# Optimization experiments

Measured on AMD Instinct MI355X. Metric: run time of the kernel, lower is better.

Reference implementation:

```python
import jax, jax.numpy as jnp
import numpy as np

T, B, H, V = 128, 32, 1024, 32000


def setup_inputs() -> dict:
    key = jax.random.key(0)
    ks = jax.random.split(key, 8)
    scale = 1.0 / np.sqrt(H)
    return {
        "input": jax.random.normal(ks[0], (T, B, H), dtype=jnp.float32),
        "hidden": jnp.zeros((B, H), dtype=jnp.float32),
        "w_ic": jax.random.uniform(ks[1], (H, H), jnp.float32, -scale, scale),
        "w_ix": jax.random.uniform(ks[2], (H, H), jnp.float32, -scale, scale),
        "w_fc": jax.random.uniform(ks[3], (H, H), jnp.float32, -scale, scale),
        "w_fx": jax.random.uniform(ks[4], (H, H), jnp.float32, -scale, scale),
        "b_i": jnp.zeros((H,), dtype=jnp.float32),
        "b_f": jnp.zeros((H,), dtype=jnp.float32),
        "W_out": jax.random.uniform(ks[5], (V, H), jnp.float32, -scale, scale),
        "b_out": jnp.zeros((V,), dtype=jnp.float32),
    }


def reference(input, hidden, w_ic, w_ix, w_fc, w_fx, b_i, b_f, W_out, b_out):
    # Precompute input projections for all timesteps: [T, B, H]
    ix = jnp.einsum("tbh,kh->tbk", input, w_ix)
    fx = jnp.einsum("tbh,kh->tbk", input, w_fx)

    def step(c, xs):
        ix_t, fx_t, x_t = xs
        i_t = jax.nn.sigmoid(c @ w_ic.T + b_i + ix_t)
        f_t = jax.nn.sigmoid(c @ w_fc.T + b_f + fx_t)
        c_new = i_t * x_t + f_t * c  # RAN gated-additive update
        return c_new, c_new

    hidden_final, outputs = jax.lax.scan(step, hidden, (ix, fx, input))
    logits = jnp.einsum("tbh,vh->tbv", outputs, W_out) + b_out
    log_probs = jax.nn.log_softmax(logits, axis=-1)
    return log_probs, hidden_final
```

## Files before the change

### kernel.cpp

```cpp
#include <hip/hip_runtime.h>

typedef __attribute__((ext_vector_type(4))) float f32x4;
typedef __attribute__((ext_vector_type(8))) short bf16x8;
typedef __attribute__((ext_vector_type(4))) unsigned u32x4;

#define T_DIM 128
#define B_DIM 32
#define H_DIM 1024
#define V_DIM 32000
#define MROWS 4096
#define NBLK 64
#define PUBSTEP 32768
#define WSTRIDE 1028
#define GBK 32

__device__ __forceinline__ ushort f2bf(float f){
  union { float f; unsigned u; } x; x.f = f;
  unsigned u = x.u;
  unsigned r = (u + 0x7fffu + ((u >> 16) & 1u)) >> 16;
  return (ushort)r;
}
__device__ __forceinline__ float bf2f(ushort h){
  union { unsigned u; float f; } x; x.u = ((unsigned)h) << 16;
  return x.f;
}

__device__ __forceinline__ void async_copy16(void* lds, const void* g){
  __builtin_amdgcn_global_load_lds((const __attribute__((address_space(1))) void*)g,
                                   (__attribute__((address_space(3))) void*)lds, 16, 0, 0);
}

__global__ void cast_bf16_kernel(const float* __restrict__ s, ushort* __restrict__ d, int n4){
  int stride = gridDim.x * blockDim.x;
  for (int i = blockIdx.x*blockDim.x + threadIdx.x; i < n4; i += stride){
    float4 v = ((const float4*)s)[i];
    ushort4 o = make_ushort4(f2bf(v.x), f2bf(v.y), f2bf(v.z), f2bf(v.w));
    ((ushort4*)d)[i] = o;
  }
}

__global__ void cast_split_kernel(const float* __restrict__ s, ushort* __restrict__ dh,
                                  ushort* __restrict__ dl, int n4){
  int stride = gridDim.x * blockDim.x;
  for (int i = blockIdx.x*blockDim.x + threadIdx.x; i < n4; i += stride){
    float4 v = ((const float4*)s)[i];
    ushort4 h = make_ushort4(f2bf(v.x), f2bf(v.y), f2bf(v.z), f2bf(v.w));
    ushort4 l = make_ushort4(f2bf(v.x - bf2f(h.x)), f2bf(v.y - bf2f(h.y)),
                             f2bf(v.z - bf2f(h.z)), f2bf(v.w - bf2f(h.w)));
    ((ushort4*)dh)[i] = h;
    ((ushort4*)dl)[i] = l;
  }
}

__global__ __launch_bounds__(256) void gemm_bt_plain(
    const ushort* __restrict__ A, const ushort* __restrict__ B,
    float* __restrict__ C, int N, int K, int NTN)
{
  __shared__ ushort lA[128*32];
  __shared__ ushort lB[128*32];
  int tid = threadIdx.x;
  int lane = tid & 63, wid = tid >> 6;
  int tm = blockIdx.x / NTN, tn = blockIdx.x % NTN;
  int row0 = tm << 7, col0 = tn << 7;

  f32x4 acc[4][4] = {};

  auto stage = [&](const ushort* __restrict__ g, ushort* l, int r0, int k0){
    int c = wid << 1;
    const ushort* s0 = g + (size_t)(r0 + (c<<4) + (lane>>2))*K + k0 + ((lane&3)<<3);
    async_copy16(l + (c<<9), s0);
    async_copy16(l + ((c+1)<<9), s0 + (size_t)16*K);
  };

  int nk = K >> 5;
  stage(A, lA, row0, 0);
  stage(B, lB, col0, 0);
  int wm = (wid >> 1) << 6, wn = (wid & 1) << 6;
  int kg = (lane >> 4) << 3;
  int ar = lane & 15;

  for (int kt = 0; kt < nk; ++kt){
    __syncthreads();
    bf16x8 af[4], bfr[4];
    #pragma unroll
    for (int mi = 0; mi < 4; ++mi) af[mi]  = *(const bf16x8*)&lA[(wm + mi*16 + ar)*32 + kg];
    #pragma unroll
    for (int ni = 0; ni < 4; ++ni) bfr[ni] = *(const bf16x8*)&lB[(wn + ni*16 + ar)*32 + kg];
    #pragma unroll
    for (int mi = 0; mi < 4; ++mi)
      #pragma unroll
      for (int ni = 0; ni < 4; ++ni)
        acc[mi][ni] = __builtin_amdgcn_mfma_f32_16x16x32_bf16(af[mi], bfr[ni], acc[mi][ni], 0, 0, 0);
    if (kt + 1 < nk){
      __syncthreads();
      stage(A, lA, row0, (kt+1) << 5);
      stage(B, lB, col0, (kt+1) << 5);
    }
  }

  int rr = (lane >> 4) << 2;
  #pragma unroll
  for (int mi = 0; mi < 4; ++mi)
    #pragma unroll
    for (int ni = 0; ni < 4; ++ni){
      int r  = row0 + wm + mi*16 + rr;
      int cc = col0 + wn + ni*16 + ar;
      #pragma unroll
      for (int q = 0; q < 4; ++q)
        C[(size_t)(r + q) * N + cc] = acc[mi][ni][q];
    }
}

__global__ __launch_bounds__(512) void gemm256(
    const ushort* __restrict__ A, const ushort* __restrict__ B,
    float* __restrict__ C, const float* __restrict__ bias,
    float* __restrict__ pmax, float* __restrict__ psum)
{
  __shared__ ushort lA[4][256*GBK];
  __shared__ ushort lB[4][256*GBK];
  __shared__ float redm[2][4][128], reds[2][4][128];

  const int K = 1024, N = V_DIM, NTN = 125, NT = 32;
  int tid = threadIdx.x, lane = tid & 63, wid = tid >> 6;
  int wm = wid >> 2, wn = wid & 3;
  int bid = blockIdx.x;
  int xcd = bid & 7, id = bid >> 3;
  int tm = (xcd << 1) | (id & 1);
  int tn = id >> 1;
  int row0 = tm << 8, col0 = tn << 8;
  int ar = lane & 15, kg = (lane >> 4) << 3;

  auto STAGE = [&](int slot, int kt){
    int k0 = kt << 5;
    #pragma unroll
    for (int j = 0; j < 2; ++j){
      int u = j*512 + tid;
      int r = u >> 2, p = u & 3;
      int g = p ^ ((r >> 1) & 3);
      int rA = row0 + r, k = k0 + (g << 3);
      const ushort* sA = A + ((size_t)(rA>>5)<<15) + ((size_t)(k>>4)<<9) + ((rA&31)<<4) + (k&15);
      async_copy16(&lA[slot][u<<3], sA);
    }
    #pragma unroll
    for (int j = 0; j < 2; ++j){
      int u = j*512 + tid;
      int r = u >> 2, p = u & 3;
      int g = p ^ ((r >> 1) & 3);
      const ushort* sB = B + (size_t)(col0 + r)*K + k0 + (g << 3);
      async_copy16(&lB[slot][u<<3], sB);
    }
  };

  f32x4 acc[8][4] = {};

  STAGE(0, 0);
  STAGE(1, 1);
  int gk = kg >> 3;
  for (int t = 0; t < NT; ++t){
    if (t + 2 < NT) STAGE((t+2) & 3, t+2);
    if (t + 2 < NT)      asm volatile("s_waitcnt vmcnt(8)" ::: "memory");
    else if (t + 1 < NT) asm volatile("s_waitcnt vmcnt(4)" ::: "memory");
    else                 asm volatile("s_waitcnt vmcnt(0)" ::: "memory");
    __builtin_amdgcn_s_barrier();
    __builtin_amdgcn_sched_barrier(0);
    const ushort* bufA = lA[t & 3];
    const ushort* bufB = lB[t & 3];
    bf16x8 a[8], b[4];
    #pragma unroll
    for (int fr = 0; fr < 8; ++fr){
      int row = wm*128 + fr*16 + ar;
      int phys = gk ^ ((row >> 1) & 3);
      a[fr] = *(const bf16x8*)&bufA[row*GBK + (phys << 3)];
    }
    #pragma unroll
    for (int fc = 0; fc < 4; ++fc){
      int row = wn*64 + fc*16 + ar;
      int phys = gk ^ ((row >> 1) & 3);
      b[fc] = *(const bf16x8*)&bufB[row*GBK + (phys << 3)];
    }
    __builtin_amdgcn_s_setprio(1);
    #pragma unroll
    for (int fr = 0; fr < 8; ++fr)
      #pragma unroll
      for (int fc = 0; fc < 4; ++fc)
        acc[fr][fc] = __builtin_amdgcn_mfma_f32_16x16x32_bf16(a[fr], b[fc], acc[fr][fc], 0, 0, 0);
    __builtin_amdgcn_s_setprio(0);
    __builtin_amdgcn_sched_barrier(0);
  }

  float bb4[4];
  #pragma unroll
  for (int fc = 0; fc < 4; ++fc) bb4[fc] = bias[col0 + wn*64 + fc*16 + ar];
  #pragma unroll
  for (int fr = 0; fr < 8; ++fr){
    #pragma unroll
    for (int q = 0; q < 4; ++q){
      int rl = fr*16 + (lane>>4)*4 + q;
      int r = row0 + wm*128 + rl;
      float vals[4];
      #pragma unroll
      for (int fc = 0; fc < 4; ++fc){
        vals[fc] = acc[fr][fc][q] + bb4[fc];
        C[(size_t)r * N + col0 + wn*64 + fc*16 + ar] = vals[fc];
      }
      float m = fmaxf(fmaxf(vals[0], vals[1]), fmaxf(vals[2], vals[3]));
      #pragma unroll
      for (int o = 1; o < 16; o <<= 1) m = fmaxf(m, __shfl_xor(m, o));
      float s = expf(vals[0]-m) + expf(vals[1]-m) + expf(vals[2]-m) + expf(vals[3]-m);
      #pragma unroll
      for (int o = 1; o < 16; o <<= 1) s += __shfl_xor(s, o);
      if (ar == 0){ redm[wm][wn][rl] = m; reds[wm][wn][rl] = s; }
    }
  }
  __syncthreads();
  if (tid < 256){
    int wm2 = tid >> 7, rl = tid & 127;
    float m0 = redm[wm2][0][rl], m1 = redm[wm2][1][rl];
    float m2 = redm[wm2][2][rl], m3 = redm[wm2][3][rl];
    float M = fmaxf(fmaxf(m0, m1), fmaxf(m2, m3));
    float S = reds[wm2][0][rl]*expf(m0-M) + reds[wm2][1][rl]*expf(m1-M)
            + reds[wm2][2][rl]*expf(m2-M) + reds[wm2][3][rl]*expf(m3-M);
    int r = row0 + wm2*128 + rl;
    pmax[(size_t)r*NTN + tn] = M;
    psum[(size_t)r*NTN + tn] = S;
  }
}

__global__ __launch_bounds__(512) void ran_all(
    unsigned* __restrict__ pub, const float* __restrict__ hiddenf,
    const ushort* __restrict__ wh, const ushort* __restrict__ wl,
    const float* __restrict__ b_i, const float* __restrict__ b_f,
    const float* __restrict__ ixfx, const float* __restrict__ x_all,
    float* __restrict__ hid_final)
{
  __shared__ ushort lWh[32*WSTRIDE];
  __shared__ ushort lWl[32*WSTRIDE];
  __shared__ f32x4 part[4][2][2][64];
  __shared__ float gsm[2*32*17];
  __shared__ float cfl[32][17];

  int tid = threadIdx.x, lane = tid & 63, wid = tid >> 6;
  int kq = wid & 3, mh = wid >> 2;
  int rgate = wid & 1, rmh = (wid >> 1) & 1;
  int bid = blockIdx.x;
  int nb = bid << 4;
  int ar = lane & 15, kg = (lane >> 4) << 3;
  int um = tid >> 4, uk = tid & 15;

  #pragma unroll
  for (int u = 0; u < 8; ++u){
    int unit = u*512 + tid;
    int r = unit >> 7, off = (unit & 127) << 3;
    int g = r >> 4, c = r & 15;
    size_t gsrc = (size_t)((g<<10) + nb + c) * H_DIM + off;
    *(bf16x8*)&lWh[r*WSTRIDE + off] = *(const bf16x8*)&wh[gsrc];
    *(bf16x8*)&lWl[r*WSTRIDE + off] = *(const bf16x8*)&wl[gsrc];
  }
  cfl[um][uk] = hiddenf[(um<<10) + nb + uk];
  float bb = (rgate ? b_f : b_i)[nb + ar];
  const ushort* b0h = &lWh[(     ar)*WSTRIDE + (kq<<8) + kg];
  const ushort* b0l = &lWl[(     ar)*WSTRIDE + (kq<<8) + kg];
  const ushort* b1h = &lWh[(16 + ar)*WSTRIDE + (kq<<8) + kg];
  const ushort* b1l = &lWl[(16 + ar)*WSTRIDE + (kq<<8) + kg];
  int abase = (kq<<13) + ((kg>>4)<<9) + (((mh<<4) + ar)<<4) + (kg & 8);
  __syncthreads();

  for (int t = 0; t < T_DIM; ++t){
    float xq1 = x_all[((size_t)t<<15) + (um<<10) + nb + uk];
    float pix[4];
    if (wid < 4){
      const float* ix_t = ixfx + ((size_t)t<<16);
      #pragma unroll
      for (int q = 0; q < 4; ++q){
        int m = (rmh<<4) + ((lane>>4)<<2) + q;
        pix[q] = ix_t[m*2048 + (rgate<<10) + nb + ar];
      }
    }

    const unsigned* ps = pub + ((size_t)t << 15) + abase;
    unsigned expt = (unsigned)(t + 1) << 16;
    u32x4 w0[8], w1[8];
    int tries = 0;
    while (1){
      #pragma unroll
      for (int f = 0; f < 8; ++f){
        const unsigned* p = ps + (f << 10);
        asm volatile("global_load_dwordx4 %0, %2, off sc0 sc1\n\t"
                     "global_load_dwordx4 %1, %2, off offset:16 sc0 sc1"
                     : "=&v"(w0[f]), "=&v"(w1[f]) : "v"(p));
      }
      asm volatile("s_waitcnt vmcnt(0)" ::: "memory");
      __builtin_amdgcn_sched_barrier(0);
      unsigned bad = 0;
      #pragma unroll
      for (int f = 0; f < 8; ++f){
        bad |= (w0[f][0]^expt)|(w0[f][1]^expt)|(w0[f][2]^expt)|(w0[f][3]^expt)
             | (w1[f][0]^expt)|(w1[f][1]^expt)|(w1[f][2]^expt)|(w1[f][3]^expt);
      }
      if (__ballot((bad & 0xFFFF0000u) != 0) == 0ull) break;
      if (++tries > (1<<15)) break;
    }

    f32x4 g0h = {}, g0l = {}, g1h = {}, g1l = {};
    #pragma unroll
    for (int f = 0; f < 8; ++f){
      union { unsigned u[4]; bf16x8 v; } cv;
      cv.u[0] = (w0[f][0] & 0xFFFFu) | (w0[f][1] << 16);
      cv.u[1] = (w0[f][2] & 0xFFFFu) | (w0[f][3] << 16);
      cv.u[2] = (w1[f][0] & 0xFFFFu) | (w1[f][1] << 16);
      cv.u[3] = (w1[f][2] & 0xFFFFu) | (w1[f][3] << 16);
      int ob = f << 5;
      bf16x8 v0h = *(const bf16x8*)&b0h[ob];
      bf16x8 v0l = *(const bf16x8*)&b0l[ob];
      bf16x8 v1h = *(const bf16x8*)&b1h[ob];
      bf16x8 v1l = *(const bf16x8*)&b1l[ob];
      g0h = __builtin_amdgcn_mfma_f32_16x16x32_bf16(cv.v, v0h, g0h, 0, 0, 0);
      g0l = __builtin_amdgcn_mfma_f32_16x16x32_bf16(cv.v, v0l, g0l, 0, 0, 0);
      g1h = __builtin_amdgcn_mfma_f32_16x16x32_bf16(cv.v, v1h, g1h, 0, 0, 0);
      g1l = __builtin_amdgcn_mfma_f32_16x16x32_bf16(cv.v, v1l, g1l, 0, 0, 0);
    }
    part[kq][mh][0][lane] = g0h + g0l;
    part[kq][mh][1][lane] = g1h + g1l;
    __syncthreads();

    if (wid < 4){
      f32x4 sum = part[0][rmh][rgate][lane] + part[1][rmh][rgate][lane]
                + part[2][rmh][rgate][lane] + part[3][rmh][rgate][lane];
      #pragma unroll
      for (int q = 0; q < 4; ++q){
        int m = (rmh<<4) + ((lane>>4)<<2) + q;
        float pre = sum[q] + bb + pix[q];
        gsm[((rgate<<5) + m)*17 + ar] = 1.f / (1.f + expf(-pre));
      }
    }
    __syncthreads();

    {
      float iv = gsm[um*17 + uk];
      float fv = gsm[(32+um)*17 + uk];
      float cv2 = cfl[um][uk];
      float cn = iv * xq1 + fv * cv2;
      cfl[um][uk] = cn;
      unsigned word = ((unsigned)(t + 2) << 16) | (unsigned)f2bf(cn);
      __hip_atomic_store(&pub[((size_t)(t+1) << 15) + (bid << 9) + tid], word,
                         __ATOMIC_RELAXED, __HIP_MEMORY_SCOPE_AGENT);
      if (t == T_DIM-1) hid_final[(um<<10) + nb + uk] = cn;
    }
    __syncthreads();
  }
}

__global__ void init_c_kernel(const float* __restrict__ hidden, unsigned* __restrict__ pub){
  int i = blockIdx.x * blockDim.x + threadIdx.x;
  float v = hidden[i];
  int m = i >> 10, col = i & 1023;
  pub[((col>>4)<<9) + (m<<4) + (col&15)] = (1u << 16) | (unsigned)f2bf(v);
}

__global__ void untag_kernel(const unsigned* __restrict__ pub, ushort* __restrict__ cst){
  int e = (blockIdx.x * blockDim.x + threadIdx.x) << 2;
  int s = e >> 15, w = e & 32767;
  const unsigned* p = pub + ((size_t)(s + 1) << 15) + w;
  ushort4 o = make_ushort4((ushort)p[0], (ushort)p[1], (ushort)p[2], (ushort)p[3]);
  *(ushort4*)&cst[e] = o;
}

__global__ __launch_bounds__(256) void subf_kernel(float* __restrict__ logits,
                                                   const float* __restrict__ pmax,
                                                   const float* __restrict__ psum){
  __shared__ float sl;
  size_t row = blockIdx.x;
  int tid = threadIdx.x;
  if (tid < 64){
    float m = -1e30f, s = 0.f;
    for (int i = tid; i < 125; i += 64){
      float mi = pmax[row*125 + i], si = psum[row*125 + i];
      float M = fmaxf(m, mi);
      s = s*expf(m - M) + si*expf(mi - M);
      m = M;
    }
    #pragma unroll
    for (int o = 32; o; o >>= 1){
      float m2 = __shfl_xor(m, o), s2 = __shfl_xor(s, o);
      float M = fmaxf(m, m2);
      s = s*expf(m - M) + s2*expf(m2 - M);
      m = M;
    }
    if (tid == 0) sl = m + logf(s);
  }
  __syncthreads();
  float l = sl;
  float4* p4 = (float4*)(logits + row * (size_t)V_DIM);
  for (int i = tid; i < V_DIM/4; i += 256){
    float4 v = p4[i];
    v.x -= l; v.y -= l; v.z -= l; v.w -= l;
    p4[i] = v;
  }
}

extern "C" void kernel_launch(void* const* d_in, const int* in_sizes, int n_in,
                              void* d_out, int out_size, void* d_ws, size_t ws_size,
                              hipStream_t stream)
{
  const float* input  = (const float*)d_in[0];
  const float* hidden = (const float*)d_in[1];
  const float* w_ic   = (const float*)d_in[2];
  const float* w_ix   = (const float*)d_in[3];
  const float* w_fc   = (const float*)d_in[4];
  const float* w_fx   = (const float*)d_in[5];
  const float* b_i    = (const float*)d_in[6];
  const float* b_f    = (const float*)d_in[7];
  const float* W_out  = (const float*)d_in[8];
  const float* b_out  = (const float*)d_in[9];
  float* out = (float*)d_out;

  char* ws = (char*)d_ws;
  ushort* wout_bf = (ushort*)(ws + 0);
  ushort* in_hi   = (ushort*)(ws + 65536000);
  ushort* wx      = (ushort*)(ws + 73924608);
  ushort* wc_hi   = (ushort*)(ws + 90701824);
  ushort* wc_lo   = (ushort*)(ws + 94896128);
  unsigned* pub   = (unsigned*)(ws + 65536000);
  ushort* cstate  = (ushort*)(ws + 82444288);
  float*  pmax    = (float*)(ws + 94896128);
  float*  psum    = (float*)(ws + 99090432);
  float*  ixfx    = out;

  cast_bf16_kernel<<<2048,256,0,stream>>>(W_out, wout_bf, V_DIM*H_DIM/4);
  cast_bf16_kernel<<<1024,256,0,stream>>>(input, in_hi, MROWS*H_DIM/4);
  cast_bf16_kernel<<<256,256,0,stream>>>(w_ix, wx,             H_DIM*H_DIM/4);
  cast_bf16_kernel<<<256,256,0,stream>>>(w_fx, wx+H_DIM*H_DIM, H_DIM*H_DIM/4);
  cast_split_kernel<<<256,256,0,stream>>>(w_ic, wc_hi,             wc_lo,             H_DIM*H_DIM/4);
  cast_split_kernel<<<256,256,0,stream>>>(w_fc, wc_hi+H_DIM*H_DIM, wc_lo+H_DIM*H_DIM, H_DIM*H_DIM/4);

  gemm_bt_plain<<<32*16,256,0,stream>>>(in_hi, wx, ixfx, 2048, H_DIM, 16);

  hipMemsetAsync(pub, 0, (size_t)129 * PUBSTEP * 4, stream);
  init_c_kernel<<<128,256,0,stream>>>(hidden, pub);

  ran_all<<<NBLK,512,0,stream>>>(pub, hidden, wc_hi, wc_lo, b_i, b_f,
                                 ixfx, input, out + (size_t)MROWS*V_DIM);

  untag_kernel<<<4096,256,0,stream>>>(pub, cstate);
  gemm256<<<2000,512,0,stream>>>(cstate, wout_bf, out, b_out, pmax, psum);
  subf_kernel<<<MROWS,256,0,stream>>>(out, pmax, psum);
}
```

Before: 1.865 ms.

## Rewrite output GEMM main loop with BK=64 quadrant ping-pong and fuse untag

```diff
diff --git a/kernel.cpp b/kernel.cpp
--- a/kernel.cpp
+++ b/kernel.cpp
@@ -12,7 +12,6 @@
 #define NBLK 64
 #define PUBSTEP 32768
 #define WSTRIDE 1028
-#define GBK 32
 
 __device__ __forceinline__ ushort f2bf(float f){
   union { float f; unsigned u; } x; x.f = f;
@@ -116,11 +115,11 @@
     float* __restrict__ C, const float* __restrict__ bias,
     float* __restrict__ pmax, float* __restrict__ psum)
 {
-  __shared__ ushort lA[4][256*GBK];
-  __shared__ ushort lB[4][256*GBK];
+  __shared__ ushort lA[2][256*64];
+  __shared__ ushort lB[2][256*64];
   __shared__ float redm[2][4][128], reds[2][4][128];
 
-  const int K = 1024, N = V_DIM, NTN = 125, NT = 32;
+  const int K = 1024, N = V_DIM, NTN = 125;
   int tid = threadIdx.x, lane = tid & 63, wid = tid >> 6;
   int wm = wid >> 2, wn = wid & 3;
   int bid = blockIdx.x;
@@ -128,65 +127,112 @@
   int tm = (xcd << 1) | (id & 1);
   int tn = id >> 1;
   int row0 = tm << 8, col0 = tn << 8;
-  int ar = lane & 15, kg = (lane >> 4) << 3;
-
-  auto STAGE = [&](int slot, int kt){
-    int k0 = kt << 5;
-    #pragma unroll
-    for (int j = 0; j < 2; ++j){
-      int u = j*512 + tid;
-      int r = u >> 2, p = u & 3;
-      int g = p ^ ((r >> 1) & 3);
-      int rA = row0 + r, k = k0 + (g << 3);
-      const ushort* sA = A + ((size_t)(rA>>5)<<15) + ((size_t)(k>>4)<<9) + ((rA&31)<<4) + (k&15);
-      async_copy16(&lA[slot][u<<3], sA);
-    }
-    #pragma unroll
-    for (int j = 0; j < 2; ++j){
-      int u = j*512 + tid;
-      int r = u >> 2, p = u & 3;
-      int g = p ^ ((r >> 1) & 3);
-      const ushort* sB = B + (size_t)(col0 + r)*K + k0 + (g << 3);
-      async_copy16(&lB[slot][u<<3], sB);
-    }
-  };
+  int ar = lane & 15, kgi = lane >> 4;
 
   f32x4 acc[8][4] = {};
-
-  STAGE(0, 0);
-  STAGE(1, 1);
-  int gk = kg >> 3;
-  for (int t = 0; t < NT; ++t){
-    if (t + 2 < NT) STAGE((t+2) & 3, t+2);
-    if (t + 2 < NT)      asm volatile("s_waitcnt vmcnt(8)" ::: "memory");
-    else if (t + 1 < NT) asm volatile("s_waitcnt vmcnt(4)" ::: "memory");
-    else                 asm volatile("s_waitcnt vmcnt(0)" ::: "memory");
-    __builtin_amdgcn_s_barrier();
-    __builtin_amdgcn_sched_barrier(0);
-    const ushort* bufA = lA[t & 3];
-    const ushort* bufB = lB[t & 3];
-    bf16x8 a[8], b[4];
-    #pragma unroll
-    for (int fr = 0; fr < 8; ++fr){
-      int row = wm*128 + fr*16 + ar;
-      int phys = gk ^ ((row >> 1) & 3);
-      a[fr] = *(const bf16x8*)&bufA[row*GBK + (phys << 3)];
-    }
-    #pragma unroll
-    for (int fc = 0; fc < 4; ++fc){
-      int row = wn*64 + fc*16 + ar;
-      int phys = gk ^ ((row >> 1) & 3);
-      b[fc] = *(const bf16x8*)&bufB[row*GBK + (phys << 3)];
-    }
-    __builtin_amdgcn_s_setprio(1);
-    #pragma unroll
-    for (int fr = 0; fr < 8; ++fr)
-      #pragma unroll
-      for (int fc = 0; fc < 4; ++fc)
-        acc[fr][fc] = __builtin_amdgcn_mfma_f32_16x16x32_bf16(a[fr], b[fc], acc[fr][fc], 0, 0, 0);
-    __builtin_amdgcn_s_setprio(0);
-    __builtin_amdgcn_sched_barrier(0);
-  }
+  bf16x8 a_[8], b_[4];
+
+#define SBAR __builtin_amdgcn_sched_barrier(0)
+#define BAR  __builtin_amdgcn_s_barrier()
+
+#define STG_A(buf, kt, h) do { \
+  _Pragma("unroll") \
+  for (int j_ = 0; j_ < 2; ++j_){ \
+    int idx_ = j_*512 + tid; \
+    int rih_ = idx_ >> 3, ps_ = idx_ & 7; \
+    int row_ = ((rih_ >> 6) << 7) | ((h) << 6) | (rih_ & 63); \
+    int g_ = ps_ ^ (row_ & 7); \
+    int kc_ = ((kt) << 6) + (g_ << 3); \
+    int rA_ = row0 + row_; \
+    const ushort* s_ = A + ((size_t)(rA_>>5)<<15) + ((size_t)(kc_>>4)<<9) + ((rA_&31)<<4) + (kc_&15); \
+    async_copy16(&lA[buf][row_*64 + ps_*8], s_); \
+  } } while(0)
+
+#define STG_B(buf, kt, h) do { \
+  _Pragma("unroll") \
+  for (int j_ = 0; j_ < 2; ++j_){ \
+    int idx_ = j_*512 + tid; \
+    int rih_ = idx_ >> 3, ps_ = idx_ & 7; \
+    int row_ = ((rih_ >> 5) << 6) | ((h) << 5) | (rih_ & 31); \
+    int g_ = ps_ ^ (row_ & 7); \
+    int kc_ = ((kt) << 6) + (g_ << 3); \
+    const ushort* s_ = B + (size_t)(col0 + row_)*K + kc_; \
+    async_copy16(&lB[buf][row_*64 + ps_*8], s_); \
+  } } while(0)
+
+#define QREAD(bsel, FRH, FCH) do { \
+  _Pragma("unroll") \
+  for (int f_ = 0; f_ < 4; ++f_) \
+    _Pragma("unroll") \
+    for (int kk_ = 0; kk_ < 2; ++kk_){ \
+      int row_ = wm*128 + ((FRH)*4 + f_)*16 + ar; \
+      int conc_ = kk_*4 + kgi; \
+      a_[f_*2+kk_] = *(const bf16x8*)&lA[bsel][row_*64 + ((conc_ ^ (row_&7))<<3)]; \
+    } \
+  _Pragma("unroll") \
+  for (int f_ = 0; f_ < 2; ++f_) \
+    _Pragma("unroll") \
+    for (int kk_ = 0; kk_ < 2; ++kk_){ \
+      int row_ = wn*64 + ((FCH)*2 + f_)*16 + ar; \
+      int conc_ = kk_*4 + kgi; \
+      b_[f_*2+kk_] = *(const bf16x8*)&lB[bsel][row_*64 + ((conc_ ^ (row_&7))<<3)]; \
+    } } while(0)
+
+#define QMFMA(FRH, FCH) do { \
+  __builtin_amdgcn_s_setprio(1); \
+  _Pragma("unroll") \
+  for (int f_ = 0; f_ < 4; ++f_) \
+    _Pragma("unroll") \
+    for (int c_ = 0; c_ < 2; ++c_) \
+      _Pragma("unroll") \
+      for (int kk_ = 0; kk_ < 2; ++kk_) \
+        acc[(FRH)*4+f_][(FCH)*2+c_] = __builtin_amdgcn_mfma_f32_16x16x32_bf16( \
+            a_[f_*2+kk_], b_[c_*2+kk_], acc[(FRH)*4+f_][(FCH)*2+c_], 0, 0, 0); \
+  __builtin_amdgcn_s_setprio(0); \
+} while(0)
+
+#define VM4 asm volatile("s_waitcnt vmcnt(4)" ::: "memory")
+#define VM0 asm volatile("s_waitcnt vmcnt(0)" ::: "memory")
+
+  STG_A(0,0,0); STG_B(0,0,0); STG_A(0,0,1); STG_B(0,0,1);
+  STG_A(1,1,0); STG_B(1,1,1);
+  VM4;
+  SBAR; BAR; SBAR;
+
+  for (int it = 0; it < 8; ++it){
+    int kO = 2*it + 1, kE2 = 2*it + 2, kO2 = 2*it + 3;
+    QREAD(0, 0, 0);
+    STG_A(1, kO, 1); STG_B(1, kO, 0);
+    SBAR; BAR; QMFMA(0, 0); SBAR; BAR; SBAR;
+    QREAD(0, 0, 1);
+    SBAR; BAR; QMFMA(0, 1); SBAR; BAR; SBAR;
+    QREAD(0, 1, 1);
+    if (it < 7) STG_A(0, kE2, 0);
+    SBAR; BAR; QMFMA(1, 1); SBAR; BAR; SBAR;
+    QREAD(0, 1, 0);
+    if (it < 7){ STG_B(0, kE2, 1); VM4; } else { VM0; }
+    SBAR; BAR; QMFMA(1, 0); SBAR; BAR; SBAR;
+    QREAD(1, 0, 0);
+    if (it < 7){ STG_A(0, kE2, 1); STG_B(0, kE2, 0); }
+    SBAR; BAR; QMFMA(0, 0); SBAR; BAR; SBAR;
+    QREAD(1, 0, 1);
+    SBAR; BAR; QMFMA(0, 1); SBAR; BAR; SBAR;
+    QREAD(1, 1, 1);
+    if (it < 7) STG_A(1, kO2, 0);
+    SBAR; BAR; QMFMA(1, 1); SBAR; BAR; SBAR;
+    QREAD(1, 1, 0);
+    if (it < 7){ STG_B(1, kO2, 1); VM4; }
+    SBAR; BAR; QMFMA(1, 0); SBAR; BAR; SBAR;
+  }
+
+#undef SBAR
+#undef BAR
+#undef STG_A
+#undef STG_B
+#undef QREAD
+#undef QMFMA
+#undef VM4
+#undef VM0
 
   float bb4[4];
   #pragma unroll
@@ -227,7 +273,8 @@
 }
 
 __global__ __launch_bounds__(512) void ran_all(
-    unsigned* __restrict__ pub, const float* __restrict__ hiddenf,
+    unsigned* __restrict__ pub, ushort* __restrict__ cst,
+    const float* __restrict__ hiddenf,
     const ushort* __restrict__ wh, const ushort* __restrict__ wl,
     const float* __restrict__ b_i, const float* __restrict__ b_f,
     const float* __restrict__ ixfx, const float* __restrict__ x_all,
@@ -341,9 +388,11 @@
       float cv2 = cfl[um][uk];
       float cn = iv * xq1 + fv * cv2;
       cfl[um][uk] = cn;
-      unsigned word = ((unsigned)(t + 2) << 16) | (unsigned)f2bf(cn);
+      ushort hb = f2bf(cn);
+      unsigned word = ((unsigned)(t + 2) << 16) | (unsigned)hb;
       __hip_atomic_store(&pub[((size_t)(t+1) << 15) + (bid << 9) + tid], word,
                          __ATOMIC_RELAXED, __HIP_MEMORY_SCOPE_AGENT);
+      cst[((size_t)t << 15) + (bid << 9) + tid] = hb;
       if (t == T_DIM-1) hid_final[(um<<10) + nb + uk] = cn;
     }
     __syncthreads();
@@ -355,14 +404,6 @@
   float v = hidden[i];
   int m = i >> 10, col = i & 1023;
   pub[((col>>4)<<9) + (m<<4) + (col&15)] = (1u << 16) | (unsigned)f2bf(v);
-}
-
-__global__ void untag_kernel(const unsigned* __restrict__ pub, ushort* __restrict__ cst){
-  int e = (blockIdx.x * blockDim.x + threadIdx.x) << 2;
-  int s = e >> 15, w = e & 32767;
-  const unsigned* p = pub + ((size_t)(s + 1) << 15) + w;
-  ushort4 o = make_ushort4((ushort)p[0], (ushort)p[1], (ushort)p[2], (ushort)p[3]);
-  *(ushort4*)&cst[e] = o;
 }
 
 __global__ __launch_bounds__(256) void subf_kernel(float* __restrict__ logits,
@@ -438,10 +479,9 @@
   hipMemsetAsync(pub, 0, (size_t)129 * PUBSTEP * 4, stream);
   init_c_kernel<<<128,256,0,stream>>>(hidden, pub);
 
-  ran_all<<<NBLK,512,0,stream>>>(pub, hidden, wc_hi, wc_lo, b_i, b_f,
+  ran_all<<<NBLK,512,0,stream>>>(pub, cstate, hidden, wc_hi, wc_lo, b_i, b_f,
                                  ixfx, input, out + (size_t)MROWS*V_DIM);
 
-  untag_kernel<<<4096,256,0,stream>>>(pub, cstate);
   gemm256<<<2000,512,0,stream>>>(cstate, wout_bf, out, b_out, pmax, psum);
   subf_kernel<<<MROWS,256,0,stream>>>(out, pmax, psum);
 }
```

After: 1.976 ms. +5.9%, slower.
